# Kernel tuning notes

Hardware: AMD Instinct MI355X
Metric: run time of the kernel (lower is better)

## Reference

```python
import jax, jax.numpy as jnp
import numpy as np

N, S, E, H = 2, 2048, 1024, 16
D = E // H


def setup_inputs() -> dict:
    key = jax.random.key(0)
    ks = jax.random.split(key, 12)
    std = 0.02
    inp = {
        "q_data": jax.random.normal(ks[0], (N, S, E), jnp.float32),
        "k_data": jax.random.normal(ks[1], (N, S, E), jnp.float32),
        "v_data": jax.random.normal(ks[2], (N, S, E), jnp.float32),
        "Wq_w": jax.random.normal(ks[3], (E, E), jnp.float32) * std,
        "Wq_b": jnp.zeros((E,), jnp.float32),
        "Wk_w": jax.random.normal(ks[4], (E, E), jnp.float32) * std,
        "Wk_b": jnp.zeros((E,), jnp.float32),
        "Wv_w": jax.random.normal(ks[5], (E, E), jnp.float32) * std,
        "Wv_b": jnp.zeros((E,), jnp.float32),
        "Wo_w": jax.random.normal(ks[6], (E, E), jnp.float32) * std,
        "Wo_b": jnp.zeros((E,), jnp.float32),
        "attn_mask": jax.random.randint(ks[7], (S, S), 0, 2, jnp.int32),
    }
    return inp


def reference(q_data, k_data, v_data, Wq_w, Wq_b, Wk_w, Wk_b, Wv_w, Wv_b, Wo_w, Wo_b, attn_mask):
    n, s, e = q_data.shape
    # projections (torch Linear: x @ W.T + b), split heads -> [N, H, S, D]
    q = (q_data @ Wq_w.T + Wq_b).reshape(n, s, H, D).transpose(0, 2, 1, 3)
    k = (k_data @ Wk_w.T + Wk_b).reshape(n, -1, H, D).transpose(0, 2, 1, 3)
    v = (v_data @ Wv_w.T + Wv_b).reshape(n, -1, H, D).transpose(0, 2, 1, 3)
    scores = jnp.einsum("bhsd,bhtd->bhst", q, k) / np.sqrt(D).astype(np.float32)
    mask = (attn_mask == 0)[None, None, :, :]  # True where masked (mask==0)
    scores = jnp.where(mask, -jnp.inf, scores)
    attn = jax.nn.softmax(scores, axis=-1)  # dropout is identity in eval mode
    out = jnp.einsum("bhst,bhtd->bhsd", attn, v)
    out = out.transpose(0, 2, 1, 3).reshape(n, s, e)
    out = out @ Wo_w.T + Wo_b
    return (out, attn)
```

## Files before the change

kernel.cpp:

```cpp
#include <hip/hip_runtime.h>

typedef __bf16 bf16x8 __attribute__((ext_vector_type(8)));
typedef float  f32x4  __attribute__((ext_vector_type(4)));
typedef unsigned short u16x8 __attribute__((ext_vector_type(8)));

static __device__ __forceinline__ unsigned short f2b(float f) {
  unsigned int u = __float_as_uint(f);
  unsigned int r = u + 0x7fffu + ((u >> 16) & 1u);
  return (unsigned short)(r >> 16);
}

__device__ __forceinline__ void gload_lds16(const void* g, void* l) {
  __builtin_amdgcn_global_load_lds(
      (const __attribute__((address_space(1))) unsigned int*)g,
      (__attribute__((address_space(3))) unsigned int*)l, 16, 0, 0);
}

constexpr int NB = 2, S = 2048, E = 1024, H = 16, D = 64;
constexpr int M = NB * S;

constexpr size_t XQ_E = 0;
constexpr size_t XK_E = 4194304;
constexpr size_t XV_E = 8388608;
constexpr size_t WQ_E = 12582912;
constexpr size_t WK_E = 13631488;
constexpr size_t WV_E = 14680064;
constexpr size_t WO_E = 15728640;
constexpr size_t MB_B = 33554432;
constexpr size_t Q_E  = 17039360;
constexpr size_t K_E  = 21233664;
constexpr size_t V_E  = 25427968;
constexpr size_t VT_E = 29622272;
constexpr size_t OP_E = 33816576;
constexpr size_t OUT0 = (size_t)M * E;

__global__ __launch_bounds__(256) void cast_all_k(
    const float* __restrict__ q, const float* __restrict__ k, const float* __restrict__ v,
    const float* __restrict__ wq, const float* __restrict__ wk,
    const float* __restrict__ wv, const float* __restrict__ wo,
    unsigned short* __restrict__ ws) {
  int a = blockIdx.y;
  const float* s; unsigned short* d; int n;
  switch (a) {
    case 0: s = q;  d = ws + XQ_E; n = M * E; break;
    case 1: s = k;  d = ws + XK_E; n = M * E; break;
    case 2: s = v;  d = ws + XV_E; n = M * E; break;
    case 3: s = wq; d = ws + WQ_E; n = E * E; break;
    case 4: s = wk; d = ws + WK_E; n = E * E; break;
    case 5: s = wv; d = ws + WV_E; n = E * E; break;
    default: s = wo; d = ws + WO_E; n = E * E; break;
  }
  int i = (blockIdx.x * 256 + threadIdx.x) * 8;
  if (i >= n) return;
  float4 f0 = *(const float4*)(s + i);
  float4 f1 = *(const float4*)(s + i + 4);
  u16x8 o;
  o[0] = f2b(f0.x); o[1] = f2b(f0.y); o[2] = f2b(f0.z); o[3] = f2b(f0.w);
  o[4] = f2b(f1.x); o[5] = f2b(f1.y); o[6] = f2b(f1.z); o[7] = f2b(f1.w);
  *(u16x8*)(d + i) = o;
}

__global__ __launch_bounds__(256) void maskbits_k(const int* __restrict__ mask,
                                                  unsigned long long* __restrict__ mbT) {
  int wid = blockIdx.x * 4 + (threadIdx.x >> 6);
  int lane = threadIdx.x & 63;
  int s = wid >> 5, wi = wid & 31;
  int v = mask[(size_t)s * S + wi * 64 + lane];
  unsigned long long b = __ballot(v != 0);
  if (lane == 0) mbT[(size_t)wi * S + s] = b;
}

template <int MODE>
__global__ __launch_bounds__(256) void gemm128_k(
    const unsigned short* __restrict__ A, const unsigned short* __restrict__ Bw,
    const float* __restrict__ bias, unsigned short* __restrict__ Cb, float* __restrict__ Cf) {
  __shared__ unsigned short As[128 * 64];
  __shared__ unsigned short Bs[128 * 64];
  const int tid = threadIdx.x, lane = tid & 63, w = tid >> 6;
  const int m0 = blockIdx.x * 128, n0 = blockIdx.y * 128;
  const int part = lane >> 4, fcol = lane & 15;
  const int wr = w >> 1, wc = w & 1;
  const int srow = lane >> 3;
  const int sg = (lane & 7) ^ (srow & 7);
  f32x4 acc[4][4] = {};
  for (int k0 = 0; k0 < E; k0 += 64) {
    __syncthreads();
#pragma unroll
    for (int c = 0; c < 4; ++c) {
      int rbase = w * 32 + c * 8;
      int row = rbase + srow;
      gload_lds16(&A[(size_t)(m0 + row) * E + k0 + sg * 8], &As[rbase * 64]);
      gload_lds16(&Bw[(size_t)(n0 + row) * E + k0 + sg * 8], &Bs[rbase * 64]);
    }
    __syncthreads();
#pragma unroll
    for (int kc = 0; kc < 2; ++kc) {
      bf16x8 af[4], bfr[4];
#pragma unroll
      for (int mi = 0; mi < 4; ++mi) {
        int r = wr * 64 + mi * 16 + fcol;
        af[mi] = *(const bf16x8*)&As[r * 64 + (((kc * 4 + part) ^ (r & 7)) * 8)];
      }
#pragma unroll
      for (int ni = 0; ni < 4; ++ni) {
        int r = wc * 64 + ni * 16 + fcol;
        bfr[ni] = *(const bf16x8*)&Bs[r * 64 + (((kc * 4 + part) ^ (r & 7)) * 8)];
      }
#pragma unroll
      for (int mi = 0; mi < 4; ++mi)
#pragma unroll
        for (int ni = 0; ni < 4; ++ni)
          acc[mi][ni] = __builtin_amdgcn_mfma_f32_16x16x32_bf16(af[mi], bfr[ni], acc[mi][ni], 0, 0, 0);
    }
  }
#pragma unroll
  for (int ni = 0; ni < 4; ++ni) {
    int e = n0 + wc * 64 + ni * 16 + fcol;
    float bv = bias[e];
#pragma unroll
    for (int mi = 0; mi < 4; ++mi) {
#pragma unroll
      for (int j = 0; j < 4; ++j) {
        int m = m0 + wr * 64 + mi * 16 + part * 4 + j;
        float val = acc[mi][ni][j] + bv;
        if (MODE == 0) {
          int nn = m >> 11, sx = m & (S - 1), hh = e >> 6, dd = e & 63;
          Cb[((size_t)(nn * H + hh) * S + sx) * D + dd] = f2b(val);
        } else {
          Cf[(size_t)m * E + e] = val;
        }
      }
    }
  }
}

__global__ __launch_bounds__(256) void vtrans_k(const unsigned short* __restrict__ V,
                                                unsigned short* __restrict__ Vt) {
  __shared__ unsigned short T[64 * 64];
  const int nh = blockIdx.y, t0 = blockIdx.x * 64;
  const unsigned short* Vh = V + (size_t)nh * S * D;
  unsigned short* Vth = Vt + (size_t)nh * D * S;
  const int tid = threadIdx.x, srow = tid >> 3, c8 = tid & 7;
#pragma unroll
  for (int rr = 0; rr < 2; ++rr) {
    int r = srow + rr * 32;
    *(u16x8*)&T[r * 64 + ((c8 ^ (r & 7)) * 8)] = *(const u16x8*)&Vh[(size_t)(t0 + r) * D + c8 * 8];
  }
  __syncthreads();
#pragma unroll
  for (int rr = 0; rr < 2; ++rr) {
    int d = srow + rr * 32;
    u16x8 o;
#pragma unroll
    for (int i = 0; i < 8; ++i) {
      int t = c8 * 8 + i;
      o[i] = T[t * 64 + (((d >> 3) ^ (t & 7)) * 8) + (d & 7)];
    }
    *(u16x8*)&Vth[(size_t)d * S + t0 + c8 * 8] = o;
  }
}

__global__ __launch_bounds__(256) void attn_k(
    const unsigned short* __restrict__ Q, const unsigned short* __restrict__ K,
    const unsigned short* __restrict__ Vt, const unsigned long long* __restrict__ mbT,
    float* __restrict__ attn_out, unsigned short* __restrict__ OP) {
  __shared__ unsigned short Qs[64 * 64];
  __shared__ unsigned short Ks[64 * 64];
  __shared__ unsigned short Vs[64 * 64];
  __shared__ unsigned short Ps[64 * 64];
  __shared__ unsigned long long Mw[64];

  const int tid = threadIdx.x, lane = tid & 63, w = tid >> 6;
  const int nh = blockIdx.y, r0 = blockIdx.x * 64;
  const unsigned short* Qh = Q + (size_t)nh * S * D;
  const unsigned short* Kh = K + (size_t)nh * S * D;
  const unsigned short* Vh = Vt + (size_t)nh * D * S;
  float* Ah = attn_out + (size_t)nh * S * S;
  const int srow = tid >> 3, c8 = tid & 7;
  const int part = lane >> 4, fcol = lane & 15;
  const int arow = 16 * w + fcol;

#pragma unroll
  for (int rr = 0; rr < 2; ++rr) {
    int r = srow + rr * 32;
    *(u16x8*)&Qs[r * 64 + ((c8 ^ (r & 7)) * 8)] = *(const u16x8*)&Qh[(size_t)(r0 + r) * D + c8 * 8];
  }
  __syncthreads();
  bf16x8 aq[2];
#pragma unroll
  for (int kc = 0; kc < 2; ++kc)
    aq[kc] = *(const bf16x8*)&Qs[arow * 64 + (((kc * 4 + part) ^ (arow & 7)) * 8)];

  float mrow[4] = {-1e30f, -1e30f, -1e30f, -1e30f};
  float lrow[4] = {0.f, 0.f, 0.f, 0.f};

  for (int t0 = 0; t0 < S; t0 += 64) {
    __syncthreads();
#pragma unroll
    for (int rr = 0; rr < 2; ++rr) {
      int r = srow + rr * 32;
      *(u16x8*)&Ks[r * 64 + ((c8 ^ (r & 7)) * 8)] = *(const u16x8*)&Kh[(size_t)(t0 + r) * D + c8 * 8];
    }
    if (tid < 64) Mw[tid] = mbT[(size_t)(t0 >> 6) * S + r0 + tid];
    __syncthreads();
    f32x4 sc[4];
#pragma unroll
    for (int cg = 0; cg < 4; ++cg) {
      f32x4 a = {0.f, 0.f, 0.f, 0.f};
#pragma unroll
      for (int kc = 0; kc < 2; ++kc) {
        int br = cg * 16 + fcol;
        bf16x8 b = *(const bf16x8*)&Ks[br * 64 + (((kc * 4 + part) ^ (br & 7)) * 8)];
        a = __builtin_amdgcn_mfma_f32_16x16x32_bf16(aq[kc], b, a, 0, 0, 0);
      }
      sc[cg] = a;
    }
#pragma unroll
    for (int j = 0; j < 4; ++j) {
      unsigned long long mw = Mw[16 * w + part * 4 + j];
      float sv[4]; float tmax = -1e30f;
#pragma unroll
      for (int cg = 0; cg < 4; ++cg) {
        int bit = cg * 16 + fcol;
        float svv = ((mw >> bit) & 1ull) ? sc[cg][j] * 0.125f : -1e30f;
        sv[cg] = svv; tmax = fmaxf(tmax, svv);
      }
#pragma unroll
      for (int xm = 1; xm < 16; xm <<= 1) tmax = fmaxf(tmax, __shfl_xor(tmax, xm));
      float mnew = fmaxf(mrow[j], tmax);
      float ps = 0.f;
#pragma unroll
      for (int cg = 0; cg < 4; ++cg) ps += __expf(sv[cg] - mnew);
#pragma unroll
      for (int xm = 1; xm < 16; xm <<= 1) ps += __shfl_xor(ps, xm);
      lrow[j] = lrow[j] * __expf(mrow[j] - mnew) + ps;
      mrow[j] = mnew;
    }
  }
  float invl[4];
#pragma unroll
  for (int j = 0; j < 4; ++j) invl[j] = 1.0f / lrow[j];

  f32x4 oacc[4] = {};

  for (int t0 = 0; t0 < S; t0 += 64) {
    __syncthreads();
#pragma unroll
    for (int rr = 0; rr < 2; ++rr) {
      int r = srow + rr * 32;
      *(u16x8*)&Ks[r * 64 + ((c8 ^ (r & 7)) * 8)] = *(const u16x8*)&Kh[(size_t)(t0 + r) * D + c8 * 8];
      *(u16x8*)&Vs[r * 64 + ((c8 ^ (r & 7)) * 8)] = *(const u16x8*)&Vh[(size_t)r * S + t0 + c8 * 8];
    }
    if (tid < 64) Mw[tid] = mbT[(size_t)(t0 >> 6) * S + r0 + tid];
    __syncthreads();
    f32x4 sc[4];
#pragma unroll
    for (int cg = 0; cg < 4; ++cg) {
      f32x4 a = {0.f, 0.f, 0.f, 0.f};
#pragma unroll
      for (int kc = 0; kc < 2; ++kc) {
        int br = cg * 16 + fcol;
        bf16x8 b = *(const bf16x8*)&Ks[br * 64 + (((kc * 4 + part) ^ (br & 7)) * 8)];
        a = __builtin_amdgcn_mfma_f32_16x16x32_bf16(aq[kc], b, a, 0, 0, 0);
      }
      sc[cg] = a;
    }
#pragma unroll
    for (int j = 0; j < 4; ++j) {
      unsigned long long mw = Mw[16 * w + part * 4 + j];
      int row = 16 * w + part * 4 + j;
#pragma unroll
      for (int cg = 0; cg < 4; ++cg) {
        int bit = cg * 16 + fcol;
        float svv = ((mw >> bit) & 1ull) ? sc[cg][j] * 0.125f : -1e30f;
        float p = __expf(svv - mrow[j]) * invl[j];
        Ah[(size_t)(r0 + row) * S + t0 + cg * 16 + fcol] = p;
        Ps[row * 64 + ((((cg * 16 + fcol) >> 3) ^ (row & 7)) * 8) + (fcol & 7)] = f2b(p);
      }
    }
#pragma unroll
    for (int kc = 0; kc < 2; ++kc) {
      bf16x8 pa = *(const bf16x8*)&Ps[arow * 64 + (((kc * 4 + part) ^ (arow & 7)) * 8)];
#pragma unroll
      for (int cg = 0; cg < 4; ++cg) {
        int vr = cg * 16 + fcol;
        bf16x8 vb = *(const bf16x8*)&Vs[vr * 64 + (((kc * 4 + part) ^ (vr & 7)) * 8)];
        oacc[cg] = __builtin_amdgcn_mfma_f32_16x16x32_bf16(pa, vb, oacc[cg], 0, 0, 0);
      }
    }
  }
  const int nn = nh >> 4, hh = nh & 15;
#pragma unroll
  for (int cg = 0; cg < 4; ++cg) {
#pragma unroll
    for (int j = 0; j < 4; ++j) {
      int row = 16 * w + part * 4 + j;
      size_t m = (size_t)nn * S + r0 + row;
      int e = hh * 64 + cg * 16 + fcol;
      OP[m * E + e] = f2b(oacc[cg][j]);
    }
  }
}

extern "C" void kernel_launch(void* const* d_in, const int* in_sizes, int n_in,
                              void* d_out, int out_size, void* d_ws, size_t ws_size,
                              hipStream_t stream) {
  (void)in_sizes; (void)n_in; (void)out_size; (void)ws_size;
  const float* q_data = (const float*)d_in[0];
  const float* k_data = (const float*)d_in[1];
  const float* v_data = (const float*)d_in[2];
  const float* Wq_w = (const float*)d_in[3];
  const float* Wq_b = (const float*)d_in[4];
  const float* Wk_w = (const float*)d_in[5];
  const float* Wk_b = (const float*)d_in[6];
  const float* Wv_w = (const float*)d_in[7];
  const float* Wv_b = (const float*)d_in[8];
  const float* Wo_w = (const float*)d_in[9];
  const float* Wo_b = (const float*)d_in[10];
  const int* attn_mask = (const int*)d_in[11];

  unsigned short* ws16 = (unsigned short*)d_ws;
  unsigned long long* mbT = (unsigned long long*)((char*)d_ws + MB_B);
  float* out_f = (float*)d_out;
  float* attn_f = out_f + OUT0;

  cast_all_k<<<dim3(2048, 7), 256, 0, stream>>>(q_data, k_data, v_data, Wq_w, Wk_w, Wv_w, Wo_w, ws16);
  maskbits_k<<<dim3(16384), 256, 0, stream>>>(attn_mask, mbT);
  gemm128_k<0><<<dim3(32, 8), 256, 0, stream>>>(ws16 + XQ_E, ws16 + WQ_E, Wq_b, ws16 + Q_E, nullptr);
  gemm128_k<0><<<dim3(32, 8), 256, 0, stream>>>(ws16 + XK_E, ws16 + WK_E, Wk_b, ws16 + K_E, nullptr);
  gemm128_k<0><<<dim3(32, 8), 256, 0, stream>>>(ws16 + XV_E, ws16 + WV_E, Wv_b, ws16 + V_E, nullptr);
  vtrans_k<<<dim3(32, 32), 256, 0, stream>>>(ws16 + V_E, ws16 + VT_E);
  attn_k<<<dim3(32, 32), 256, 0, stream>>>(ws16 + Q_E, ws16 + K_E, ws16 + VT_E, mbT, attn_f, ws16 + OP_E);
  gemm128_k<1><<<dim3(32, 8), 256, 0, stream>>>(ws16 + OP_E, ws16 + WO_E, Wo_b, nullptr, out_f);
}
```

Baseline: 859.5 us.

## Drop softmax max tracking, batch QKV GEMMs, use direct global-to-LDS loads

```diff
diff --git a/kernel.cpp b/kernel.cpp
--- a/kernel.cpp
+++ b/kernel.cpp
@@ -18,6 +18,8 @@
 
 constexpr int NB = 2, S = 2048, E = 1024, H = 16, D = 64;
 constexpr int M = NB * S;
+
+constexpr float SC = 0.125f * 1.44269504088896f;
 
 constexpr size_t XQ_E = 0;
 constexpr size_t XK_E = 4194304;
@@ -71,13 +73,12 @@
 }
 
 template <int MODE>
-__global__ __launch_bounds__(256) void gemm128_k(
+__device__ __forceinline__ void gemm128_body(
     const unsigned short* __restrict__ A, const unsigned short* __restrict__ Bw,
-    const float* __restrict__ bias, unsigned short* __restrict__ Cb, float* __restrict__ Cf) {
-  __shared__ unsigned short As[128 * 64];
-  __shared__ unsigned short Bs[128 * 64];
+    const float* __restrict__ bias, unsigned short* __restrict__ Cb,
+    float* __restrict__ Cf, int m0, int n0,
+    unsigned short* As, unsigned short* Bs) {
   const int tid = threadIdx.x, lane = tid & 63, w = tid >> 6;
-  const int m0 = blockIdx.x * 128, n0 = blockIdx.y * 128;
   const int part = lane >> 4, fcol = lane & 15;
   const int wr = w >> 1, wc = w & 1;
   const int srow = lane >> 3;
@@ -134,6 +135,27 @@
   }
 }
 
+__global__ __launch_bounds__(256) void gemm_qkv_k(
+    unsigned short* __restrict__ ws,
+    const float* __restrict__ bq, const float* __restrict__ bk, const float* __restrict__ bv) {
+  __shared__ unsigned short As[128 * 64];
+  __shared__ unsigned short Bs[128 * 64];
+  const int z = blockIdx.z;
+  const unsigned short* A  = ws + XQ_E + (size_t)z * ((size_t)M * E);
+  const unsigned short* Bw = ws + WQ_E + (size_t)z * ((size_t)E * E);
+  unsigned short* Cb       = ws + Q_E  + (size_t)z * ((size_t)M * E);
+  const float* bias = (z == 0) ? bq : ((z == 1) ? bk : bv);
+  gemm128_body<0>(A, Bw, bias, Cb, nullptr, blockIdx.x * 128, blockIdx.y * 128, As, Bs);
+}
+
+__global__ __launch_bounds__(256) void gemm_o_k(
+    const unsigned short* __restrict__ A, const unsigned short* __restrict__ Bw,
+    const float* __restrict__ bias, float* __restrict__ Cf) {
+  __shared__ unsigned short As[128 * 64];
+  __shared__ unsigned short Bs[128 * 64];
+  gemm128_body<1>(A, Bw, bias, nullptr, Cf, blockIdx.x * 128, blockIdx.y * 128, As, Bs);
+}
+
 __global__ __launch_bounds__(256) void vtrans_k(const unsigned short* __restrict__ V,
                                                 unsigned short* __restrict__ Vt) {
   __shared__ unsigned short T[64 * 64];
@@ -176,14 +198,15 @@
   const unsigned short* Kh = K + (size_t)nh * S * D;
   const unsigned short* Vh = Vt + (size_t)nh * D * S;
   float* Ah = attn_out + (size_t)nh * S * S;
-  const int srow = tid >> 3, c8 = tid & 7;
   const int part = lane >> 4, fcol = lane & 15;
   const int arow = 16 * w + fcol;
-
-#pragma unroll
-  for (int rr = 0; rr < 2; ++rr) {
-    int r = srow + rr * 32;
-    *(u16x8*)&Qs[r * 64 + ((c8 ^ (r & 7)) * 8)] = *(const u16x8*)&Qh[(size_t)(r0 + r) * D + c8 * 8];
+  const int srow8 = lane >> 3;
+  const int sg = (lane & 7) ^ (srow8 & 7);
+
+#pragma unroll
+  for (int c = 0; c < 2; ++c) {
+    int rbase = w * 16 + c * 8;
+    gload_lds16(&Qh[(size_t)(r0 + rbase + srow8) * D + sg * 8], &Qs[rbase * 64]);
   }
   __syncthreads();
   bf16x8 aq[2];
@@ -191,15 +214,14 @@
   for (int kc = 0; kc < 2; ++kc)
     aq[kc] = *(const bf16x8*)&Qs[arow * 64 + (((kc * 4 + part) ^ (arow & 7)) * 8)];
 
-  float mrow[4] = {-1e30f, -1e30f, -1e30f, -1e30f};
   float lrow[4] = {0.f, 0.f, 0.f, 0.f};
 
   for (int t0 = 0; t0 < S; t0 += 64) {
     __syncthreads();
 #pragma unroll
-    for (int rr = 0; rr < 2; ++rr) {
-      int r = srow + rr * 32;
-      *(u16x8*)&Ks[r * 64 + ((c8 ^ (r & 7)) * 8)] = *(const u16x8*)&Kh[(size_t)(t0 + r) * D + c8 * 8];
+    for (int c = 0; c < 2; ++c) {
+      int rbase = w * 16 + c * 8;
+      gload_lds16(&Kh[(size_t)(t0 + rbase + srow8) * D + sg * 8], &Ks[rbase * 64]);
     }
     if (tid < 64) Mw[tid] = mbT[(size_t)(t0 >> 6) * S + r0 + tid];
     __syncthreads();
@@ -218,23 +240,16 @@
 #pragma unroll
     for (int j = 0; j < 4; ++j) {
       unsigned long long mw = Mw[16 * w + part * 4 + j];
-      float sv[4]; float tmax = -1e30f;
+      float ps = 0.f;
 #pragma unroll
       for (int cg = 0; cg < 4; ++cg) {
         int bit = cg * 16 + fcol;
-        float svv = ((mw >> bit) & 1ull) ? sc[cg][j] * 0.125f : -1e30f;
-        sv[cg] = svv; tmax = fmaxf(tmax, svv);
-      }
-#pragma unroll
-      for (int xm = 1; xm < 16; xm <<= 1) tmax = fmaxf(tmax, __shfl_xor(tmax, xm));
-      float mnew = fmaxf(mrow[j], tmax);
-      float ps = 0.f;
-#pragma unroll
-      for (int cg = 0; cg < 4; ++cg) ps += __expf(sv[cg] - mnew);
+        float e = exp2f(sc[cg][j] * SC);
+        ps += ((mw >> bit) & 1ull) ? e : 0.f;
+      }
 #pragma unroll
       for (int xm = 1; xm < 16; xm <<= 1) ps += __shfl_xor(ps, xm);
-      lrow[j] = lrow[j] * __expf(mrow[j] - mnew) + ps;
-      mrow[j] = mnew;
+      lrow[j] += ps;
     }
   }
   float invl[4];
@@ -246,10 +261,10 @@
   for (int t0 = 0; t0 < S; t0 += 64) {
     __syncthreads();
 #pragma unroll
-    for (int rr = 0; rr < 2; ++rr) {
-      int r = srow + rr * 32;
-      *(u16x8*)&Ks[r * 64 + ((c8 ^ (r & 7)) * 8)] = *(const u16x8*)&Kh[(size_t)(t0 + r) * D + c8 * 8];
-      *(u16x8*)&Vs[r * 64 + ((c8 ^ (r & 7)) * 8)] = *(const u16x8*)&Vh[(size_t)r * S + t0 + c8 * 8];
+    for (int c = 0; c < 2; ++c) {
+      int rbase = w * 16 + c * 8;
+      gload_lds16(&Kh[(size_t)(t0 + rbase + srow8) * D + sg * 8], &Ks[rbase * 64]);
+      gload_lds16(&Vh[(size_t)(rbase + srow8) * S + t0 + sg * 8], &Vs[rbase * 64]);
     }
     if (tid < 64) Mw[tid] = mbT[(size_t)(t0 >> 6) * S + r0 + tid];
     __syncthreads();
@@ -272,8 +287,8 @@
 #pragma unroll
       for (int cg = 0; cg < 4; ++cg) {
         int bit = cg * 16 + fcol;
-        float svv = ((mw >> bit) & 1ull) ? sc[cg][j] * 0.125f : -1e30f;
-        float p = __expf(svv - mrow[j]) * invl[j];
+        float e = exp2f(sc[cg][j] * SC) * invl[j];
+        float p = ((mw >> bit) & 1ull) ? e : 0.f;
         Ah[(size_t)(r0 + row) * S + t0 + cg * 16 + fcol] = p;
         Ps[row * 64 + ((((cg * 16 + fcol) >> 3) ^ (row & 7)) * 8) + (fcol & 7)] = f2b(p);
       }
@@ -309,11 +324,8 @@
   const float* q_data = (const float*)d_in[0];
   const float* k_data = (const float*)d_in[1];
   const float* v_data = (const float*)d_in[2];
-  const float* Wq_w = (const float*)d_in[3];
   const float* Wq_b = (const float*)d_in[4];
-  const float* Wk_w = (const float*)d_in[5];
   const float* Wk_b = (const float*)d_in[6];
-  const float* Wv_w = (const float*)d_in[7];
   const float* Wv_b = (const float*)d_in[8];
   const float* Wo_w = (const float*)d_in[9];
   const float* Wo_b = (const float*)d_in[10];
@@ -324,12 +336,12 @@
   float* out_f = (float*)d_out;
   float* attn_f = out_f + OUT0;
 
-  cast_all_k<<<dim3(2048, 7), 256, 0, stream>>>(q_data, k_data, v_data, Wq_w, Wk_w, Wv_w, Wo_w, ws16);
+  cast_all_k<<<dim3(2048, 7), 256, 0, stream>>>(q_data, k_data, v_data,
+                                                (const float*)d_in[3], (const float*)d_in[5],
+                                                (const float*)d_in[7], Wo_w, ws16);
   maskbits_k<<<dim3(16384), 256, 0, stream>>>(attn_mask, mbT);
-  gemm128_k<0><<<dim3(32, 8), 256, 0, stream>>>(ws16 + XQ_E, ws16 + WQ_E, Wq_b, ws16 + Q_E, nullptr);
-  gemm128_k<0><<<dim3(32, 8), 256, 0, stream>>>(ws16 + XK_E, ws16 + WK_E, Wk_b, ws16 + K_E, nullptr);
-  gemm128_k<0><<<dim3(32, 8), 256, 0, stream>>>(ws16 + XV_E, ws16 + WV_E, Wv_b, ws16 + V_E, nullptr);
+  gemm_qkv_k<<<dim3(32, 8, 3), 256, 0, stream>>>(ws16, Wq_b, Wk_b, Wv_b);
   vtrans_k<<<dim3(32, 32), 256, 0, stream>>>(ws16 + V_E, ws16 + VT_E);
   attn_k<<<dim3(32, 32), 256, 0, stream>>>(ws16 + Q_E, ws16 + K_E, ws16 + VT_E, mbT, attn_f, ws16 + OP_E);
-  gemm128_k<1><<<dim3(32, 8), 256, 0, stream>>>(ws16 + OP_E, ws16 + WO_E, Wo_b, nullptr, out_f);
-}
+  gemm_o_k<<<dim3(32, 8), 256, 0, stream>>>(ws16 + OP_E, ws16 + WO_E, Wo_b, out_f);
+}
```

Result: faster. 842.3 us (-2.0%).
